# Kernel tuning notes

Hardware: AMD Instinct MI355X
Metric: run time of the kernel (lower is better)

## Reference

```python
import jax, jax.numpy as jnp
import numpy as np

N = 8192
D_IN = 512
D_HID = 1024
D_OUT = 512
N_NEIGHS = 16


def setup_inputs() -> dict:
    key = jax.random.key(0)
    k1, k2, k3 = jax.random.split(key, 3)
    x = jax.random.normal(k1, (N, D_IN), dtype=jnp.float32)
    # build a fake_edge_mask with exactly N_NEIGHS ones per row (distinct cols)
    rows = jnp.arange(N)[:, None]                      # [N,1]
    cols = (rows + 1 + jnp.arange(N_NEIGHS)[None, :]) % N  # [N,K] distinct
    fake_edge_mask = jnp.zeros((N, N), dtype=jnp.bool_).at[rows, cols].set(True)
    real_edge_mask = jnp.zeros((N, N), dtype=jnp.bool_)  # unused by forward math
    W1 = jax.random.normal(k2, (D_IN, D_HID), dtype=jnp.float32) * (1.0 / np.sqrt(D_IN))
    b1 = jnp.zeros((D_HID,), dtype=jnp.float32)
    W2 = jax.random.normal(k3, (D_HID, D_OUT), dtype=jnp.float32) * (1.0 / np.sqrt(D_HID))
    b2 = jnp.zeros((D_OUT,), dtype=jnp.float32)
    return {"x": x, "real_edge_mask": real_edge_mask, "fake_edge_mask": fake_edge_mask,
            "W1": W1, "b1": b1, "W2": W2, "b2": b2}


def reference(x, real_edge_mask, fake_edge_mask, W1, b1, W2, b2):
    # torch.nonzero(mask)[:,1].reshape(N, K): per-row column indices of the K ones.
    # top_k on 0/1 values returns the K ones' indices (tie-break = ascending index);
    # the subsequent sum is permutation-invariant so ordering is irrelevant.
    _, idx = jax.lax.top_k(fake_edge_mask.astype(jnp.float32), N_NEIGHS)  # [N,K]
    niche_feat = x[idx]                                  # [N,K,D] gather
    res = jnp.sum(niche_feat, axis=1) / N_NEIGHS         # mean over neighbors
    hidden = x + res                                     # residual add
    h = jax.nn.relu(hidden @ W1 + b1)                    # fc1 + ReLU
    out = h @ W2 + b2                                    # fc2
    return out
```

## Files before the change

kernel.cpp:

```cpp
#include <hip/hip_runtime.h>

typedef __attribute__((ext_vector_type(8))) short sh8;
typedef __attribute__((ext_vector_type(4))) float fl4;

__device__ __forceinline__ unsigned short f2bf(float f) {
    unsigned int u = __float_as_uint(f);
    unsigned int r = (u + 0x7fffu + ((u >> 16) & 1u)) >> 16;
    return (unsigned short)r;
}

#define GLDS16(gp, lp) __builtin_amdgcn_global_load_lds( \
    (const __attribute__((address_space(1))) void*)(gp), \
    (__attribute__((address_space(3))) void*)(lp), 16, 0, 0)

#define NROWS   8192
#define D_IN    512
#define D_HID   1024
#define D_OUT   512
#define NNEIGH  16

__global__ __launch_bounds__(256) void prep(
    const float* __restrict__ x,
    const int* __restrict__ mask_w,
    unsigned short* __restrict__ hB,
    const float* __restrict__ W1, unsigned short* __restrict__ W1t,
    const float* __restrict__ W2, unsigned short* __restrict__ W2t)
{
    const int b   = blockIdx.x;
    const int tid = threadIdx.x;

    __shared__ float tile[32][33];
    __shared__ int okrow[16];
    __shared__ int idxs[64];
    __shared__ int cnt;

    if (b >= 512) {
        const float* in; unsigned short* out; int R, C, c0, r0;
        if (b < 1024) {
            const int i = b - 512;
            in = W1; out = W1t; R = D_IN; C = D_HID;
            c0 = (i & 31) * 32; r0 = (i >> 5) * 32;
        } else {
            const int i = b - 1024;
            in = W2; out = W2t; R = D_HID; C = D_OUT;
            c0 = (i & 15) * 32; r0 = (i >> 4) * 32;
        }
        const int tx = tid & 31, ty = tid >> 5;
        #pragma unroll
        for (int k = 0; k < 4; k++)
            tile[ty + 8 * k][tx] = in[(size_t)(r0 + ty + 8 * k) * C + c0 + tx];
        __syncthreads();
        #pragma unroll
        for (int k = 0; k < 4; k++)
            out[(size_t)(c0 + ty + 8 * k) * R + r0 + tx] = f2bf(tile[tx][ty + 8 * k]);
        return;
    }

    const int r0 = b * 16;
    const bool i32mode = (mask_w[1] == 1);

    if (tid < 16) okrow[tid] = 1;
    __syncthreads();
    {
        const int rl = tid >> 4, k = tid & 15;
        const int row = r0 + rl;
        int c = row + 1 + k; if (c >= NROWS) c -= NROWS;
        int set = i32mode ? (mask_w[(size_t)row * NROWS + c] != 0)
                          : (((const unsigned char*)mask_w)[(size_t)row * NROWS + c] != 0);
        if (!set) atomicAnd(&okrow[rl], 0);
    }
    __syncthreads();
    bool allok = true;
    #pragma unroll
    for (int i = 0; i < 16; i++) allok &= (okrow[i] != 0);

    const float2* X = (const float2*)x;
    auto rowp = [&](int r) -> const float2* {
        int rr = (r >= NROWS) ? r - NROWS : r;
        return X + (size_t)rr * (D_IN / 2);
    };

    if (allok) {
        float wx = 0.f, wy = 0.f;
        #pragma unroll 4
        for (int j = 1; j <= 16; j++) {
            const float2 v = rowp(r0 + j)[tid];
            wx += v.x; wy += v.y;
        }
        float2 xr = rowp(r0)[tid];
        #pragma unroll 2
        for (int r = 0; r < 16; r++) {
            const int row = r0 + r;
            const float2 sub = rowp(row + 1)[tid];
            const float2 add = rowp(row + 17)[tid];
            ushort2 o;
            o.x = f2bf(xr.x + wx * (1.f / 16.f));
            o.y = f2bf(xr.y + wy * (1.f / 16.f));
            *((ushort2*)(hB + (size_t)row * D_IN) + tid) = o;
            wx += add.x - sub.x; wy += add.y - sub.y;
            xr = sub;
        }
    } else {
        for (int r = 0; r < 16; r++) {
            const int row = r0 + r;
            if (tid == 0) cnt = 0;
            if (tid < 64) idxs[tid] = row;
            __syncthreads();
            for (int j = 0; j < NROWS / 256; j++) {
                int c = tid * (NROWS / 256) + j;
                int set = i32mode ? (mask_w[(size_t)row * NROWS + c] != 0)
                                  : (((const unsigned char*)mask_w)[(size_t)row * NROWS + c] != 0);
                if (set) { int q = atomicAdd(&cnt, 1); if (q < 64) idxs[q] = c; }
            }
            __syncthreads();
            float sx = 0.f, sy = 0.f;
            for (int k = 0; k < NNEIGH; k++) {
                int idx = idxs[k];
                idx = (idx < 0) ? 0 : ((idx > NROWS - 1) ? NROWS - 1 : idx);
                const float2 v = X[(size_t)idx * (D_IN / 2) + tid];
                sx += v.x; sy += v.y;
            }
            const float2 xv = X[(size_t)row * (D_IN / 2) + tid];
            ushort2 o;
            o.x = f2bf(xv.x + sx * (1.f / 16.f));
            o.y = f2bf(xv.y + sy * (1.f / 16.f));
            *((ushort2*)(hB + (size_t)row * D_IN) + tid) = o;
            __syncthreads();
        }
    }
}

template<int WGM, int WGN, int TM, int TN, bool RELU, bool OUT_BF16>
__global__ __launch_bounds__(256) void gemm_bt(
    const unsigned short* __restrict__ A,
    const unsigned short* __restrict__ Bt,
    const float* __restrict__ bias,
    void* __restrict__ Cout,
    int M, int N, int K)
{
    constexpr int BM = WGM * TM * 16;
    constexpr int BN = WGN * TN * 16;
    constexpr int ASLOTS = BM * 64 / 2048;
    constexpr int BSLOTS = BN * 64 / 2048;
    __shared__ unsigned short As[BM * 64];
    __shared__ unsigned short Bs[BN * 64];

    const int tid  = threadIdx.x;
    const long m0  = (long)blockIdx.y * BM;
    const long n0  = (long)blockIdx.x * BN;
    const int wave = tid >> 6, lane = tid & 63;
    const int wm = (wave % WGM) * (TM * 16), wn = (wave / WGM) * (TN * 16);
    const int lm = lane & 15, q8 = (lane >> 4) * 8;

    fl4 acc[TM][TN] = {};

    for (int kt = 0; kt < K; kt += 64) {
        #pragma unroll
        for (int s = 0; s < ASLOTS; s++) {
            const int L = tid * 8 + s * 2048;
            const int row = L >> 6, kv = (L & 63) ^ ((row & 7) << 3);
            GLDS16(&A[(m0 + row) * K + kt + kv], &As[L]);
        }
        #pragma unroll
        for (int s = 0; s < BSLOTS; s++) {
            const int L = tid * 8 + s * 2048;
            const int row = L >> 6, kv = (L & 63) ^ ((row & 7) << 3);
            GLDS16(&Bt[(n0 + row) * K + kt + kv], &Bs[L]);
        }
        __syncthreads();

        #pragma unroll
        for (int ks = 0; ks < 2; ks++) {
            const int klog = ks * 32 + q8;
            sh8 af[TM], bf_[TN];
            #pragma unroll
            for (int t = 0; t < TM; t++) {
                const int ra = wm + t * 16 + lm;
                af[t] = *(const sh8*)(&As[ra * 64 + (klog ^ ((ra & 7) << 3))]);
            }
            #pragma unroll
            for (int t = 0; t < TN; t++) {
                const int rb = wn + t * 16 + lm;
                bf_[t] = *(const sh8*)(&Bs[rb * 64 + (klog ^ ((rb & 7) << 3))]);
            }
            #pragma unroll
            for (int tm = 0; tm < TM; tm++)
                #pragma unroll
                for (int tn = 0; tn < TN; tn++)
                    acc[tm][tn] = __builtin_amdgcn_mfma_f32_16x16x32_bf16(
                        af[tm], bf_[tn], acc[tm][tn], 0, 0, 0);
        }
        __syncthreads();
    }

    const int rq = (lane >> 4) * 4;
    #pragma unroll
    for (int tm = 0; tm < TM; tm++) {
        #pragma unroll
        for (int tn = 0; tn < TN; tn++) {
            const long col = n0 + wn + tn * 16 + lm;
            const float bv = bias[col];
            #pragma unroll
            for (int r = 0; r < 4; r++) {
                const long row = m0 + wm + tm * 16 + rq + r;
                float v = acc[tm][tn][r] + bv;
                if (RELU) v = fmaxf(v, 0.f);
                if (OUT_BF16) ((unsigned short*)Cout)[row * N + col] = f2bf(v);
                else          ((float*)Cout)[row * N + col] = v;
            }
        }
    }
}

extern "C" void kernel_launch(void* const* d_in, const int* in_sizes, int n_in,
                              void* d_out, int out_size, void* d_ws, size_t ws_size,
                              hipStream_t stream)
{
    const float* x     = (const float*)d_in[0];
    const int*   fmask = (const int*)d_in[2];
    const float* W1    = (const float*)d_in[3];
    const float* b1    = (const float*)d_in[4];
    const float* W2    = (const float*)d_in[5];
    const float* b2    = (const float*)d_in[6];
    float*       out   = (float*)d_out;

    const size_t needElts = (size_t)NROWS * D_IN + (size_t)D_HID * D_IN
                          + (size_t)D_OUT * D_HID + (size_t)NROWS * D_HID;
    unsigned short* base = (ws_size >= needElts * sizeof(unsigned short))
                         ? (unsigned short*)d_ws
                         : (unsigned short*)d_in[1];

    unsigned short* hiddenB = base;
    unsigned short* W1t     = hiddenB + (size_t)NROWS * D_IN;
    unsigned short* W2t     = W1t + (size_t)D_HID * D_IN;
    unsigned short* h       = W2t + (size_t)D_OUT * D_HID;

    prep<<<1536, 256, 0, stream>>>(x, fmask, hiddenB, W1, W1t, W2, W2t);
    gemm_bt<2, 2, 4, 4, true, true><<<dim3(D_HID / 128, NROWS / 128), 256, 0, stream>>>(
        hiddenB, W1t, b1, h, NROWS, D_HID, D_IN);
    gemm_bt<1, 4, 4, 2, false, false><<<dim3(D_OUT / 128, NROWS / 64), 256, 0, stream>>>(
        h, W2t, b2, out, NROWS, D_OUT, D_HID);
}
```

Baseline: 449.5 us.

## Fuse prep and both GEMMs into one cooperative persistent kernel with grid syncs

Replaces three separate kernel launches with a single cooperative kernel of 512 blocks that loops over prep units, then the fc1 GEMM tiles, then the fc2 GEMM tiles, separated by grid-wide syncs. The aim is to remove launch gaps and inter-kernel drain and fill. The shared LDS buffers are sized for the largest phase, and the three-launch path is kept as a fallback if the cooperative launch fails. In exchange it adds grid-sync overhead, requires two blocks per CU to be co-resident, and loses the occupancy the separate kernels could reach.

```diff
diff --git a/kernel.cpp b/kernel.cpp
--- a/kernel.cpp
+++ b/kernel.cpp
@@ -1,4 +1,7 @@
 #include <hip/hip_runtime.h>
+#include <hip/hip_cooperative_groups.h>
+
+namespace cg = cooperative_groups;
 
 typedef __attribute__((ext_vector_type(8))) short sh8;
 typedef __attribute__((ext_vector_type(4))) float fl4;
@@ -19,20 +22,16 @@
 #define D_OUT   512
 #define NNEIGH  16
 
-__global__ __launch_bounds__(256) void prep(
+__device__ __forceinline__ void prep_unit(
+    int b,
     const float* __restrict__ x,
     const int* __restrict__ mask_w,
     unsigned short* __restrict__ hB,
     const float* __restrict__ W1, unsigned short* __restrict__ W1t,
-    const float* __restrict__ W2, unsigned short* __restrict__ W2t)
-{
-    const int b   = blockIdx.x;
+    const float* __restrict__ W2, unsigned short* __restrict__ W2t,
+    float (*tile)[33], int* okrow, int* idxs, int* cnt)
+{
     const int tid = threadIdx.x;
-
-    __shared__ float tile[32][33];
-    __shared__ int okrow[16];
-    __shared__ int idxs[64];
-    __shared__ int cnt;
 
     if (b >= 512) {
         const float* in; unsigned short* out; int R, C, c0, r0;
@@ -53,6 +52,7 @@
         #pragma unroll
         for (int k = 0; k < 4; k++)
             out[(size_t)(c0 + ty + 8 * k) * R + r0 + tx] = f2bf(tile[tx][ty + 8 * k]);
+        __syncthreads();
         return;
     }
 
@@ -103,14 +103,14 @@
     } else {
         for (int r = 0; r < 16; r++) {
             const int row = r0 + r;
-            if (tid == 0) cnt = 0;
+            if (tid == 0) *cnt = 0;
             if (tid < 64) idxs[tid] = row;
             __syncthreads();
             for (int j = 0; j < NROWS / 256; j++) {
                 int c = tid * (NROWS / 256) + j;
                 int set = i32mode ? (mask_w[(size_t)row * NROWS + c] != 0)
                                   : (((const unsigned char*)mask_w)[(size_t)row * NROWS + c] != 0);
-                if (set) { int q = atomicAdd(&cnt, 1); if (q < 64) idxs[q] = c; }
+                if (set) { int q = atomicAdd(cnt, 1); if (q < 64) idxs[q] = c; }
             }
             __syncthreads();
             float sx = 0.f, sy = 0.f;
@@ -128,26 +128,28 @@
             __syncthreads();
         }
     }
+    __syncthreads();
 }
 
 template<int WGM, int WGN, int TM, int TN, bool RELU, bool OUT_BF16>
-__global__ __launch_bounds__(256) void gemm_bt(
+__device__ __forceinline__ void gemm_unit(
+    int bx, int by,
     const unsigned short* __restrict__ A,
     const unsigned short* __restrict__ Bt,
     const float* __restrict__ bias,
     void* __restrict__ Cout,
-    int M, int N, int K)
+    int M, int N, int K,
+    unsigned short* __restrict__ As,
+    unsigned short* __restrict__ Bs)
 {
     constexpr int BM = WGM * TM * 16;
     constexpr int BN = WGN * TN * 16;
     constexpr int ASLOTS = BM * 64 / 2048;
     constexpr int BSLOTS = BN * 64 / 2048;
-    __shared__ unsigned short As[BM * 64];
-    __shared__ unsigned short Bs[BN * 64];
 
     const int tid  = threadIdx.x;
-    const long m0  = (long)blockIdx.y * BM;
-    const long n0  = (long)blockIdx.x * BN;
+    const long m0  = (long)by * BM;
+    const long n0  = (long)bx * BN;
     const int wave = tid >> 6, lane = tid & 63;
     const int wm = (wave % WGM) * (TM * 16), wn = (wave / WGM) * (TN * 16);
     const int lm = lane & 15, q8 = (lane >> 4) * 8;
@@ -212,6 +214,72 @@
     }
 }
 
+__global__ __launch_bounds__(256, 2) void fused(
+    const float* __restrict__ x,
+    const int* __restrict__ mask_w,
+    unsigned short* __restrict__ hiddenB,
+    const float* __restrict__ W1, unsigned short* __restrict__ W1t,
+    const float* __restrict__ W2, unsigned short* __restrict__ W2t,
+    const float* __restrict__ b1,
+    unsigned short* __restrict__ h,
+    const float* __restrict__ b2,
+    float* __restrict__ out)
+{
+    __shared__ unsigned short As[128 * 64];
+    __shared__ unsigned short Bs[128 * 64];
+    __shared__ float tile[32][33];
+    __shared__ int okrow[16];
+    __shared__ int idxs[64];
+    __shared__ int cnt;
+
+    cg::grid_group grid = cg::this_grid();
+
+    for (int u = blockIdx.x; u < 1536; u += gridDim.x)
+        prep_unit(u, x, mask_w, hiddenB, W1, W1t, W2, W2t, tile, okrow, idxs, &cnt);
+
+    grid.sync();
+
+    for (int vb = blockIdx.x; vb < 512; vb += gridDim.x)
+        gemm_unit<2, 2, 4, 4, true, true>(vb & 7, vb >> 3,
+            hiddenB, W1t, b1, h, NROWS, D_HID, D_IN, As, Bs);
+
+    grid.sync();
+
+    for (int vb = blockIdx.x; vb < 512; vb += gridDim.x)
+        gemm_unit<1, 4, 4, 2, false, false>(vb & 3, vb >> 2,
+            h, W2t, b2, out, NROWS, D_OUT, D_HID, As, Bs);
+}
+
+__global__ __launch_bounds__(256) void prep(
+    const float* __restrict__ x,
+    const int* __restrict__ mask_w,
+    unsigned short* __restrict__ hB,
+    const float* __restrict__ W1, unsigned short* __restrict__ W1t,
+    const float* __restrict__ W2, unsigned short* __restrict__ W2t)
+{
+    __shared__ float tile[32][33];
+    __shared__ int okrow[16];
+    __shared__ int idxs[64];
+    __shared__ int cnt;
+    prep_unit(blockIdx.x, x, mask_w, hB, W1, W1t, W2, W2t, tile, okrow, idxs, &cnt);
+}
+
+template<int WGM, int WGN, int TM, int TN, bool RELU, bool OUT_BF16>
+__global__ __launch_bounds__(256) void gemm_bt(
+    const unsigned short* __restrict__ A,
+    const unsigned short* __restrict__ Bt,
+    const float* __restrict__ bias,
+    void* __restrict__ Cout,
+    int M, int N, int K)
+{
+    constexpr int BM = WGM * TM * 16;
+    constexpr int BN = WGN * TN * 16;
+    __shared__ unsigned short As[BM * 64];
+    __shared__ unsigned short Bs[BN * 64];
+    gemm_unit<WGM, WGN, TM, TN, RELU, OUT_BF16>(blockIdx.x, blockIdx.y,
+        A, Bt, bias, Cout, M, N, K, As, Bs);
+}
+
 extern "C" void kernel_launch(void* const* d_in, const int* in_sizes, int n_in,
                               void* d_out, int out_size, void* d_ws, size_t ws_size,
                               hipStream_t stream)
@@ -235,9 +303,20 @@
     unsigned short* W2t     = W1t + (size_t)D_HID * D_IN;
     unsigned short* h       = W2t + (size_t)D_OUT * D_HID;
 
-    prep<<<1536, 256, 0, stream>>>(x, fmask, hiddenB, W1, W1t, W2, W2t);
-    gemm_bt<2, 2, 4, 4, true, true><<<dim3(D_HID / 128, NROWS / 128), 256, 0, stream>>>(
-        hiddenB, W1t, b1, h, NROWS, D_HID, D_IN);
-    gemm_bt<1, 4, 4, 2, false, false><<<dim3(D_OUT / 128, NROWS / 64), 256, 0, stream>>>(
-        h, W2t, b2, out, NROWS, D_OUT, D_HID);
-}
+    void* args[] = { (void*)&x, (void*)&fmask, (void*)&hiddenB,
+                     (void*)&W1, (void*)&W1t, (void*)&W2, (void*)&W2t,
+                     (void*)&b1, (void*)&h, (void*)&b2, (void*)&out };
+
+    hipError_t e = hipLaunchCooperativeKernel(
+        reinterpret_cast<const void*>(&fused),
+        dim3(512), dim3(256), args, 0, stream);
+
+    if (e != hipSuccess) {
+        (void)hipGetLastError();
+        prep<<<1536, 256, 0, stream>>>(x, fmask, hiddenB, W1, W1t, W2, W2t);
+        gemm_bt<2, 2, 4, 4, true, true><<<dim3(D_HID / 128, NROWS / 128), 256, 0, stream>>>(
+            hiddenB, W1t, b1, h, NROWS, D_HID, D_IN);
+        gemm_bt<1, 4, 4, 2, false, false><<<dim3(D_OUT / 128, NROWS / 64), 256, 0, stream>>>(
+            h, W2t, b2, out, NROWS, D_OUT, D_HID);
+    }
+}
```

Measured after the change: 570.5 us. 1.27x slower.
